# Optimization experiments

Measured on AMD Instinct MI355X. Metric: run time of the kernel, lower is better.

The kernel has to match this reference:

```python
import jax, jax.numpy as jnp
import numpy as np

EPS = 1e-12
RANK = 16


def setup_inputs() -> dict:
    key = jax.random.key(0)
    ks = jax.random.split(key, 7)
    bs, seq, d_in, d_out = 8, 2048, 4096, 4096
    n_tasks, n_splits, n_skills, rank = 256, 1, 8, RANK
    return {
        "x": jax.random.normal(ks[0], (bs, seq, d_in), dtype=jnp.float32),
        "task_ids": jax.random.randint(ks[1], (bs,), 0, n_tasks, dtype=jnp.int64 if jax.config.jax_enable_x64 else jnp.int32),
        "weight": jax.random.normal(ks[2], (d_out, d_in), dtype=jnp.float32) * 0.02,
        "bias": jax.random.normal(ks[3], (d_out,), dtype=jnp.float32) * 0.02,
        "module_logits": jax.random.normal(ks[4], (n_tasks, n_splits * n_skills), dtype=jnp.float32) * 0.001,
        "lora_a": jax.random.normal(ks[5], (n_splits, n_skills, d_in // n_splits, rank), dtype=jnp.float32) * 0.01,
        "lora_b": jax.random.normal(ks[6], (n_splits, n_skills, rank, d_out // n_splits), dtype=jnp.float32) * 0.01,
    }


def reference(x, task_ids, weight, bias, module_logits, lora_a, lora_b):
    bs = x.shape[0]
    n_splits, n_skills, _, rank = lora_a.shape
    d_in = n_splits * lora_a.shape[2]
    d_out = n_splits * lora_b.shape[3]
    # PolytroponSelector (eval path): sigmoid then sum-normalize over skills
    logits = module_logits[task_ids].reshape(bs, n_splits, n_skills)
    mw = jax.nn.sigmoid(logits)
    mw = mw / (mw.sum(axis=-1, keepdims=True) + EPS)  # [b, q, s]
    # Mix LoRA skill matrices per example
    A = jnp.einsum('bqs,qsdr->bqdr', mw, lora_a).reshape(bs, d_in, rank)
    B = jnp.einsum('bqs,qsrd->bqrd', mw, lora_b)
    B = jnp.transpose(B, (0, 2, 1, 3)).reshape(bs, rank, d_out)
    adapter_out = jnp.einsum('btr,brd->btd', jnp.einsum('bti,bir->btr', x, A), B) / rank
    base = jnp.einsum('bti,oi->bto', x, weight) + bias
    return base + adapter_out
```

## Files before the change

### kernel.cpp

```cpp
#include <hip/hip_runtime.h>
#include <hip/hip_bf16.h>
#include <cstdint>
#include <cstddef>

typedef __bf16 bf16_t;
typedef __bf16 bf16x8 __attribute__((ext_vector_type(8)));
typedef float f32x4 __attribute__((ext_vector_type(4)));

#define GLP(p)  (const __attribute__((address_space(1))) void*)(p)
#define LDSP(p) (__attribute__((address_space(3))) void*)(p)

static constexpr int BS   = 8;
static constexpr int SEQ  = 2048;
static constexpr int DIN  = 4096;
static constexpr int DOUT = 4096;
static constexpr int NSK  = 8;
static constexpr int RANK = 16;
static constexpr int MTOT = BS * SEQ;
static constexpr int NKT  = 128;

static __device__ __forceinline__ bf16x8 cvt8(float4 v0, float4 v1) {
    bf16x8 o;
    o[0] = (bf16_t)v0.x; o[1] = (bf16_t)v0.y; o[2] = (bf16_t)v0.z; o[3] = (bf16_t)v0.w;
    o[4] = (bf16_t)v1.x; o[5] = (bf16_t)v1.y; o[6] = (bf16_t)v1.z; o[7] = (bf16_t)v1.w;
    return o;
}

__global__ __launch_bounds__(256) void mix_kernel(
    const float* __restrict__ logits, const int* __restrict__ task_ids,
    const float* __restrict__ lora_a, const float* __restrict__ lora_b,
    bf16_t* __restrict__ Abt, bf16_t* __restrict__ Btp) {
    int b = blockIdx.y;
    int c = blockIdx.x;
    int tid = threadIdx.x;

    int t = task_ids[b];
    float w[NSK]; float sum = 0.f;
#pragma unroll
    for (int s = 0; s < NSK; ++s) {
        float lg = logits[t * NSK + s];
        float sg = 1.f / (1.f + __expf(-lg));
        w[s] = sg; sum += sg;
    }
    float inv = 1.f / (sum + 1e-12f);
#pragma unroll
    for (int s = 0; s < NSK; ++s) w[s] *= inv;

    {
        int r = tid & 15, kk = tid >> 4;
#pragma unroll
        for (int i = 0; i < 4; ++i) {
            int k = c * 64 + i * 16 + kk;
            float acc = 0.f;
#pragma unroll
            for (int s = 0; s < NSK; ++s)
                acc += w[s] * lora_a[((size_t)s * DIN + k) * RANK + r];
            Abt[((size_t)b * RANK + r) * DIN + k] = (bf16_t)acc;
        }
    }
    {
        int n = c * 64 + (tid & 63);
        int r0 = tid >> 6;
#pragma unroll
        for (int i = 0; i < 4; ++i) {
            int rr = r0 + i * 4;
            float acc = 0.f;
#pragma unroll
            for (int s = 0; s < NSK; ++s)
                acc += w[s] * lora_b[((size_t)s * RANK + rr) * DOUT + n];
            Btp[((size_t)b * DOUT + n) * 32 + rr] = (bf16_t)acc;
            Btp[((size_t)b * DOUT + n) * 32 + 16 + rr] = (bf16_t)0.f;
        }
    }
}

__global__ __launch_bounds__(256) void convw_kernel(const float* __restrict__ W,
                                                    bf16_t* __restrict__ Wb) {
    size_t g = (size_t)blockIdx.x * 256 + threadIdx.x;
    const float4* src = (const float4*)W;
    float4 v0 = src[g * 2], v1 = src[g * 2 + 1];
    *(bf16x8*)(Wb + g * 8) = cvt8(v0, v1);
}

template<bool XPRE>
__global__ __launch_bounds__(256) void tconv_kernel(
    const float* __restrict__ x, const bf16_t* __restrict__ Abt,
    bf16_t* __restrict__ xb, bf16_t* __restrict__ tpad) {
    __shared__ __align__(16) bf16_t As[64 * 64];
    __shared__ __align__(16) bf16_t Aa[16 * 64];

    int row0 = blockIdx.x * 64;
    int b = row0 >> 11;
    int tid = threadIdx.x;
    int w = tid >> 6, l = tid & 63;
    const bf16_t* Ab = Abt + (size_t)b * RANK * DIN;

    f32x4 acc = {0.f, 0.f, 0.f, 0.f};

    for (int k0 = 0; k0 < DIN; k0 += 64) {
#pragma unroll
        for (int i = 0; i < 2; ++i) {
            int flat = i * 256 + tid;
            int row = flat >> 3, c8 = flat & 7;
            const float* src = x + (size_t)(row0 + row) * DIN + k0 + c8 * 8;
            float4 v0 = *(const float4*)src;
            float4 v1 = *(const float4*)(src + 4);
            bf16x8 o = cvt8(v0, v1);
            *(bf16x8*)(&As[flat * 8]) = o;
            if (XPRE)
                *(bf16x8*)(xb + (size_t)(row0 + row) * DIN + k0 + c8 * 8) = o;
        }
        if (tid < 128) {
            int r = tid >> 3, c8 = tid & 7;
            __builtin_amdgcn_global_load_lds(GLP(Ab + (size_t)r * DIN + k0 + c8 * 8),
                                             LDSP(&Aa[tid * 8]), 16, 0, 0);
        }
        __syncthreads();
#pragma unroll
        for (int s = 0; s < 2; ++s) {
            int kr = s * 32 + (l >> 4) * 8;
            bf16x8 a = *(const bf16x8*)(&As[(w * 16 + (l & 15)) * 64 + kr]);
            bf16x8 bb = *(const bf16x8*)(&Aa[(l & 15) * 64 + kr]);
            acc = __builtin_amdgcn_mfma_f32_16x16x32_bf16(a, bb, acc, 0, 0, 0);
        }
        __syncthreads();
    }
    int r = l & 15;
    int rowb = w * 16 + (l >> 4) * 4;
#pragma unroll
    for (int j = 0; j < 4; ++j) {
        int gm = row0 + rowb + j;
        tpad[(size_t)gm * 32 + r] = (bf16_t)(acc[j] * 0.0625f);
        tpad[(size_t)gm * 32 + 16 + r] = (bf16_t)0.f;
    }
}

#define SBAR   __builtin_amdgcn_s_barrier()
#define SCHEDB __builtin_amdgcn_sched_barrier(0)
#define VMG(TXT) asm volatile("s_waitcnt " TXT ::: "memory")

__global__ __launch_bounds__(256, 2) void gemm3_kernel(
    const bf16_t* __restrict__ xb, const bf16_t* __restrict__ Wb,
    const float* __restrict__ bias,
    const bf16_t* __restrict__ tpad, const bf16_t* __restrict__ Btp,
    float* __restrict__ out) {
    __shared__ __align__(16) bf16_t lds[2][12288];

    int tid = threadIdx.x;
    int w = tid >> 6, l = tid & 63;
    int wm = w >> 1, wn = w & 1;
    int l4 = l >> 4, l15 = l & 15;

    int orig = blockIdx.x;
    int id = (orig & 7) * 256 + (orig >> 3);
    int mb = id >> 5, nb = id & 31;
    int row0 = mb * 256, col0 = nb * 128;
    int b = row0 >> 11;

    f32x4 acc[8][4] = {};

    auto stageA = [&](const bf16_t* base, size_t rstride, int c) {
#pragma unroll
        for (int ld = 0; ld < 4; ++ld) {
            int flat = ld * 256 + tid;
            int r = flat >> 2, ch = flat & 3;
            int sc = ch ^ (r & 3);
            __builtin_amdgcn_global_load_lds(
                GLP(base + (size_t)r * rstride + sc * 8),
                LDSP(&lds[c][flat * 8]), 16, 0, 0);
        }
    };
    auto stageB = [&](const bf16_t* base, size_t rstride, int c) {
#pragma unroll
        for (int ld = 0; ld < 2; ++ld) {
            int flat = ld * 256 + tid;
            int r = flat >> 2, ch = flat & 3;
            int sc = ch ^ (r & 3);
            __builtin_amdgcn_global_load_lds(
                GLP(base + (size_t)r * rstride + sc * 8),
                LDSP(&lds[c][8192 + flat * 8]), 16, 0, 0);
        }
    };

    auto loadAfrag = [&](int c, int i) {
        int row = wm * 128 + i * 16 + l15;
        return *(const bf16x8*)(&lds[c][row * 32 + ((l4 ^ (row & 3)) << 3)]);
    };
    auto loadBfrag = [&](int c, int jj) {
        int row = wn * 64 + jj * 16 + l15;
        return *(const bf16x8*)(&lds[c][8192 + row * 32 + ((l4 ^ (row & 3)) << 3)]);
    };

    const bf16_t* Abase = xb + (size_t)row0 * DIN;
    const bf16_t* Bbase = Wb + (size_t)col0 * DIN;
    const bf16_t* AbaseAdp = tpad + (size_t)row0 * 32;
    const bf16_t* BbaseAdp = Btp + ((size_t)b * DOUT + col0) * 32;

    stageA(Abase, DIN, 0);
    stageB(Bbase, DIN, 0);

#pragma unroll 1
    for (int j = 0; j <= NKT; ++j) {
        int c = j & 1;
        SCHEDB; SBAR; SCHEDB;
        if (j < NKT) {
            int jn = j + 1;
            if (jn < NKT) stageA(Abase + jn * 32, DIN, c ^ 1);
            else          stageA(AbaseAdp, 32, c ^ 1);
            VMG("vmcnt(4)");
        } else {
            VMG("vmcnt(0)");
        }
        SCHEDB;
        SBAR; SCHEDB;

        bf16x8 a0[4], a1[4], b0[2], b1[2];
#pragma unroll
        for (int i = 0; i < 4; ++i) a0[i] = loadAfrag(c, i);
#pragma unroll
        for (int jj = 0; jj < 2; ++jj) b0[jj] = loadBfrag(c, jj);
        if (j < NKT) {
            int jn = j + 1;
            if (jn < NKT) stageB(Bbase + jn * 32, DIN, c ^ 1);
            else          stageB(BbaseAdp, 32, c ^ 1);
        }
#pragma unroll
        for (int i = 0; i < 4; ++i)
#pragma unroll
            for (int jj = 0; jj < 2; ++jj)
                acc[i][jj] = __builtin_amdgcn_mfma_f32_16x16x32_bf16(
                    a0[i], b0[jj], acc[i][jj], 0, 0, 0);
#pragma unroll
        for (int jj = 0; jj < 2; ++jj) b1[jj] = loadBfrag(c, 2 + jj);
#pragma unroll
        for (int i = 0; i < 4; ++i)
#pragma unroll
            for (int jj = 0; jj < 2; ++jj)
                acc[i][2 + jj] = __builtin_amdgcn_mfma_f32_16x16x32_bf16(
                    a0[i], b1[jj], acc[i][2 + jj], 0, 0, 0);
#pragma unroll
        for (int i = 0; i < 4; ++i) a1[i] = loadAfrag(c, 4 + i);
#pragma unroll
        for (int i = 0; i < 4; ++i)
#pragma unroll
            for (int jj = 0; jj < 2; ++jj)
                acc[4 + i][2 + jj] = __builtin_amdgcn_mfma_f32_16x16x32_bf16(
                    a1[i], b1[jj], acc[4 + i][2 + jj], 0, 0, 0);
#pragma unroll
        for (int i = 0; i < 4; ++i)
#pragma unroll
            for (int jj = 0; jj < 2; ++jj)
                acc[4 + i][jj] = __builtin_amdgcn_mfma_f32_16x16x32_bf16(
                    a1[i], b0[jj], acc[4 + i][jj], 0, 0, 0);
    }

#pragma unroll
    for (int i = 0; i < 8; ++i) {
        int gm = row0 + wm * 128 + i * 16 + l4 * 4;
#pragma unroll
        for (int jj = 0; jj < 4; ++jj) {
            int gn = col0 + wn * 64 + jj * 16 + l15;
            float bsv = bias[gn];
#pragma unroll
            for (int q = 0; q < 4; ++q)
                out[(size_t)(gm + q) * DOUT + gn] = acc[i][jj][q] + bsv;
        }
    }
}

template<bool WPRE>
__global__ __launch_bounds__(256) void gemm_kernel(
    const float* __restrict__ xf,
    const float* __restrict__ Wf, const bf16_t* __restrict__ Wb,
    const float* __restrict__ bias,
    const bf16_t* __restrict__ tpad, const bf16_t* __restrict__ Btp,
    float* __restrict__ out) {
    __shared__ __align__(16) bf16_t As[128 * 64];
    __shared__ __align__(16) bf16_t Bs[128 * 64];

    int orig = blockIdx.x;
    int id = (orig & 7) * 512 + (orig >> 3);
    int mb = id >> 5, nb = id & 31;
    int row0 = mb * 128, col0 = nb * 128;
    int b = row0 >> 11;

    int tid = threadIdx.x;
    int w = tid >> 6, l = tid & 63;
    int wm = w >> 1, wn = w & 1;

    f32x4 acc[4][4] = {};

    for (int k0 = 0; k0 < DIN; k0 += 64) {
#pragma unroll
        for (int i = 0; i < 4; ++i) {
            int flat = i * 256 + tid;
            int row = flat >> 3, c8 = flat & 7;
            const float* src = xf + (size_t)(row0 + row) * DIN + k0 + c8 * 8;
            float4 v0 = *(const float4*)src;
            float4 v1 = *(const float4*)(src + 4);
            *(bf16x8*)(&As[flat * 8]) = cvt8(v0, v1);
        }
        if constexpr (WPRE) {
#pragma unroll
            for (int i = 0; i < 4; ++i) {
                int flat = i * 256 + tid;
                int row = flat >> 3, c8 = flat & 7;
                __builtin_amdgcn_global_load_lds(
                    GLP(Wb + (size_t)(col0 + row) * DIN + k0 + c8 * 8),
                    LDSP(&Bs[flat * 8]), 16, 0, 0);
            }
        } else {
#pragma unroll
            for (int i = 0; i < 4; ++i) {
                int flat = i * 256 + tid;
                int row = flat >> 3, c8 = flat & 7;
                const float* src = Wf + (size_t)(col0 + row) * DIN + k0 + c8 * 8;
                float4 v0 = *(const float4*)src;
                float4 v1 = *(const float4*)(src + 4);
                *(bf16x8*)(&Bs[flat * 8]) = cvt8(v0, v1);
            }
        }
        __syncthreads();
#pragma unroll
        for (int s = 0; s < 2; ++s) {
            int kr = s * 32 + (l >> 4) * 8;
            bf16x8 a[4], bf[4];
#pragma unroll
            for (int i = 0; i < 4; ++i)
                a[i] = *(const bf16x8*)(&As[(wm * 64 + i * 16 + (l & 15)) * 64 + kr]);
#pragma unroll
            for (int j = 0; j < 4; ++j)
                bf[j] = *(const bf16x8*)(&Bs[(wn * 64 + j * 16 + (l & 15)) * 64 + kr]);
#pragma unroll
            for (int i = 0; i < 4; ++i)
#pragma unroll
                for (int j = 0; j < 4; ++j)
                    acc[i][j] = __builtin_amdgcn_mfma_f32_16x16x32_bf16(a[i], bf[j], acc[i][j], 0, 0, 0);
        }
        __syncthreads();
    }

    {
#pragma unroll
        for (int i = 0; i < 2; ++i) {
            int flat = i * 256 + tid;
            int row = flat >> 2, c8 = flat & 3;
            __builtin_amdgcn_global_load_lds(
                GLP(tpad + (size_t)(row0 + row) * 32 + c8 * 8),
                LDSP(&As[flat * 8]), 16, 0, 0);
            __builtin_amdgcn_global_load_lds(
                GLP(Btp + ((size_t)b * DOUT + col0 + row) * 32 + c8 * 8),
                LDSP(&Bs[flat * 8]), 16, 0, 0);
        }
        __syncthreads();
        int kr = (l >> 4) * 8;
        bf16x8 a[4], bf[4];
#pragma unroll
        for (int i = 0; i < 4; ++i)
            a[i] = *(const bf16x8*)(&As[(wm * 64 + i * 16 + (l & 15)) * 32 + kr]);
#pragma unroll
        for (int j = 0; j < 4; ++j)
            bf[j] = *(const bf16x8*)(&Bs[(wn * 64 + j * 16 + (l & 15)) * 32 + kr]);
#pragma unroll
        for (int i = 0; i < 4; ++i)
#pragma unroll
            for (int j = 0; j < 4; ++j)
                acc[i][j] = __builtin_amdgcn_mfma_f32_16x16x32_bf16(a[i], bf[j], acc[i][j], 0, 0, 0);
    }

#pragma unroll
    for (int i = 0; i < 4; ++i) {
        int gm = row0 + wm * 64 + i * 16 + (l >> 4) * 4;
#pragma unroll
        for (int j = 0; j < 4; ++j) {
            int gn = col0 + wn * 64 + j * 16 + (l & 15);
            float bs = bias[gn];
#pragma unroll
            for (int q = 0; q < 4; ++q)
                out[(size_t)(gm + q) * DOUT + gn] = acc[i][j][q] + bs;
        }
    }
}

extern "C" void kernel_launch(void* const* d_in, const int* in_sizes, int n_in,
                              void* d_out, int out_size, void* d_ws, size_t ws_size,
                              hipStream_t stream) {
    const float* x        = (const float*)d_in[0];
    const int*   task_ids = (const int*)d_in[1];
    const float* W        = (const float*)d_in[2];
    const float* bias     = (const float*)d_in[3];
    const float* logits   = (const float*)d_in[4];
    const float* lora_a   = (const float*)d_in[5];
    const float* lora_b   = (const float*)d_in[6];
    float* out = (float*)d_out;

    char* ws = (char*)d_ws;
    size_t off = 0;
    auto alloc = [&](size_t bytes) {
        char* p = ws + off;
        off += (bytes + 255) & ~(size_t)255;
        return p;
    };
    bf16_t* Abt  = (bf16_t*)alloc((size_t)BS * RANK * DIN * 2);
    bf16_t* Btp  = (bf16_t*)alloc((size_t)BS * DOUT * 32 * 2);
    bf16_t* tpad = (bf16_t*)alloc((size_t)MTOT * 32 * 2);
    bf16_t* Wb   = (bf16_t*)alloc((size_t)DOUT * DIN * 2);
    size_t w_end = off;
    bf16_t* xb   = (bf16_t*)alloc((size_t)MTOT * DIN * 2);
    size_t full_end = off;

    bool wpre = ws_size >= w_end;
    bool xpre = ws_size >= full_end;

    mix_kernel<<<dim3(64, 8), 256, 0, stream>>>(logits, task_ids, lora_a, lora_b, Abt, Btp);
    if (wpre)
        convw_kernel<<<(DOUT * DIN / 8) / 256, 256, 0, stream>>>(W, Wb);
    if (xpre)
        tconv_kernel<true><<<MTOT / 64, 256, 0, stream>>>(x, Abt, xb, tpad);
    else
        tconv_kernel<false><<<MTOT / 64, 256, 0, stream>>>(x, Abt, nullptr, tpad);

    if (xpre) {
        int nblk = (MTOT / 256) * (DOUT / 128);
        gemm3_kernel<<<nblk, 256, 0, stream>>>(xb, Wb, bias, tpad, Btp, out);
    } else {
        int nblk = (MTOT / 128) * (DOUT / 128);
        if (wpre)
            gemm_kernel<true><<<nblk, 256, 0, stream>>>(x, W, Wb, bias, tpad, Btp, out);
        else
            gemm_kernel<false><<<nblk, 256, 0, stream>>>(x, W, Wb, bias, tpad, Btp, out);
    }
}
```

Before: 687.0 us.

## Restructure main GEMM to 512 threads, BK=64, triple-buffered LDS pipeline

The bf16 GEMM kernel goes from 256 to 512 threads per block, so each wave holds a 64x64 sub-tile instead of 128x64. The K step doubles to 64 with an 8-chunk XOR swizzle, and a three-deep LDS ring replaces the double buffer, with loads issued two stages ahead. The adapter rank pass becomes a separate epilogue MFMA step. The aim is to halve the barriers per K, hide more global latency and lower per-thread register pressure, at the cost of more LDS (about 144KB per block), which may limit occupancy to one block per CU.

```diff
diff --git a/kernel.cpp b/kernel.cpp
--- a/kernel.cpp
+++ b/kernel.cpp
@@ -17,7 +17,6 @@
 static constexpr int NSK  = 8;
 static constexpr int RANK = 16;
 static constexpr int MTOT = BS * SEQ;
-static constexpr int NKT  = 128;
 
 static __device__ __forceinline__ bf16x8 cvt8(float4 v0, float4 v1) {
     bf16x8 o;
@@ -139,12 +138,13 @@
 #define SCHEDB __builtin_amdgcn_sched_barrier(0)
 #define VMG(TXT) asm volatile("s_waitcnt " TXT ::: "memory")
 
-__global__ __launch_bounds__(256, 2) void gemm3_kernel(
+__global__ __launch_bounds__(512, 2) void gemm3_kernel(
     const bf16_t* __restrict__ xb, const bf16_t* __restrict__ Wb,
     const float* __restrict__ bias,
     const bf16_t* __restrict__ tpad, const bf16_t* __restrict__ Btp,
     float* __restrict__ out) {
-    __shared__ __align__(16) bf16_t lds[2][12288];
+    __shared__ __align__(16) bf16_t bufA[3][256 * 64];
+    __shared__ __align__(16) bf16_t bufB[3][128 * 64];
 
     int tid = threadIdx.x;
     int w = tid >> 6, l = tid & 63;
@@ -157,106 +157,156 @@
     int row0 = mb * 256, col0 = nb * 128;
     int b = row0 >> 11;
 
-    f32x4 acc[8][4] = {};
-
-    auto stageA = [&](const bf16_t* base, size_t rstride, int c) {
+    f32x4 acc[4][4] = {};
+
+    const bf16_t* aSrc[4];
+    const bf16_t* bSrc[2];
+#pragma unroll
+    for (int ld = 0; ld < 4; ++ld) {
+        int flat = ld * 512 + tid;
+        int r = flat >> 3;
+        int sc = (flat & 7) ^ (r & 7);
+        aSrc[ld] = xb + (size_t)(row0 + r) * DIN + sc * 8;
+    }
+#pragma unroll
+    for (int ld = 0; ld < 2; ++ld) {
+        int flat = ld * 512 + tid;
+        int r = flat >> 3;
+        int sc = (flat & 7) ^ (r & 7);
+        bSrc[ld] = Wb + (size_t)(col0 + r) * DIN + sc * 8;
+    }
+
+    auto stage = [&](int t) {
+        int c = t % 3;
+        int k0 = t * 64;
 #pragma unroll
         for (int ld = 0; ld < 4; ++ld) {
-            int flat = ld * 256 + tid;
-            int r = flat >> 2, ch = flat & 3;
-            int sc = ch ^ (r & 3);
+            int flat = ld * 512 + tid;
+            __builtin_amdgcn_global_load_lds(GLP(aSrc[ld] + k0),
+                                             LDSP(&bufA[c][flat * 8]), 16, 0, 0);
+        }
+#pragma unroll
+        for (int ld = 0; ld < 2; ++ld) {
+            int flat = ld * 512 + tid;
+            __builtin_amdgcn_global_load_lds(GLP(bSrc[ld] + k0),
+                                             LDSP(&bufB[c][flat * 8]), 16, 0, 0);
+        }
+    };
+    auto stageAdp = [&]() {
+#pragma unroll
+        for (int ld = 0; ld < 2; ++ld) {
+            int flat = ld * 512 + tid;
+            int r = flat >> 2, c4 = flat & 3;
             __builtin_amdgcn_global_load_lds(
-                GLP(base + (size_t)r * rstride + sc * 8),
-                LDSP(&lds[c][flat * 8]), 16, 0, 0);
+                GLP(tpad + (size_t)(row0 + r) * 32 + c4 * 8),
+                LDSP(&bufA[1][flat * 8]), 16, 0, 0);
+        }
+        {
+            int r = tid >> 2, c4 = tid & 3;
+            __builtin_amdgcn_global_load_lds(
+                GLP(Btp + ((size_t)b * DOUT + col0 + r) * 32 + c4 * 8),
+                LDSP(&bufB[1][tid * 8]), 16, 0, 0);
         }
     };
-    auto stageB = [&](const bf16_t* base, size_t rstride, int c) {
-#pragma unroll
-        for (int ld = 0; ld < 2; ++ld) {
-            int flat = ld * 256 + tid;
-            int r = flat >> 2, ch = flat & 3;
-            int sc = ch ^ (r & 3);
-            __builtin_amdgcn_global_load_lds(
-                GLP(base + (size_t)r * rstride + sc * 8),
-                LDSP(&lds[c][8192 + flat * 8]), 16, 0, 0);
-        }
+
+    auto loadAfrag = [&](int c, int i, int s) {
+        int row = wm * 64 + i * 16 + l15;
+        int ch = (s * 4 + l4) ^ (row & 7);
+        return *(const bf16x8*)(&bufA[c][row * 64 + ch * 8]);
     };
-
-    auto loadAfrag = [&](int c, int i) {
-        int row = wm * 128 + i * 16 + l15;
-        return *(const bf16x8*)(&lds[c][row * 32 + ((l4 ^ (row & 3)) << 3)]);
+    auto loadBfrag = [&](int c, int jj, int s) {
+        int row = wn * 64 + jj * 16 + l15;
+        int ch = (s * 4 + l4) ^ (row & 7);
+        return *(const bf16x8*)(&bufB[c][row * 64 + ch * 8]);
     };
-    auto loadBfrag = [&](int c, int jj) {
-        int row = wn * 64 + jj * 16 + l15;
-        return *(const bf16x8*)(&lds[c][8192 + row * 32 + ((l4 ^ (row & 3)) << 3)]);
-    };
-
-    const bf16_t* Abase = xb + (size_t)row0 * DIN;
-    const bf16_t* Bbase = Wb + (size_t)col0 * DIN;
-    const bf16_t* AbaseAdp = tpad + (size_t)row0 * 32;
-    const bf16_t* BbaseAdp = Btp + ((size_t)b * DOUT + col0) * 32;
-
-    stageA(Abase, DIN, 0);
-    stageB(Bbase, DIN, 0);
+
+    stage(0);
+    stage(1);
 
 #pragma unroll 1
-    for (int j = 0; j <= NKT; ++j) {
-        int c = j & 1;
+    for (int j = 0; j < 64; ++j) {
+        int c = j % 3;
         SCHEDB; SBAR; SCHEDB;
-        if (j < NKT) {
-            int jn = j + 1;
-            if (jn < NKT) stageA(Abase + jn * 32, DIN, c ^ 1);
-            else          stageA(AbaseAdp, 32, c ^ 1);
-            VMG("vmcnt(4)");
-        } else {
-            VMG("vmcnt(0)");
-        }
+        if (j < 62)       stage(j + 2);
+        else if (j == 62) stageAdp();
+        if (j < 63) { VMG("vmcnt(6)"); } else { VMG("vmcnt(3)"); }
         SCHEDB;
-        SBAR; SCHEDB;
-
-        bf16x8 a0[4], a1[4], b0[2], b1[2];
-#pragma unroll
-        for (int i = 0; i < 4; ++i) a0[i] = loadAfrag(c, i);
-#pragma unroll
-        for (int jj = 0; jj < 2; ++jj) b0[jj] = loadBfrag(c, jj);
-        if (j < NKT) {
-            int jn = j + 1;
-            if (jn < NKT) stageB(Bbase + jn * 32, DIN, c ^ 1);
-            else          stageB(BbaseAdp, 32, c ^ 1);
+
+        bf16x8 aL[2][2], aH[2][2], bL[2][2], bH[2][2];
+#pragma unroll
+        for (int i = 0; i < 2; ++i)
+#pragma unroll
+            for (int s = 0; s < 2; ++s) aL[i][s] = loadAfrag(c, i, s);
+#pragma unroll
+        for (int jj = 0; jj < 2; ++jj)
+#pragma unroll
+            for (int s = 0; s < 2; ++s) bL[jj][s] = loadBfrag(c, jj, s);
+#pragma unroll
+        for (int s = 0; s < 2; ++s)
+#pragma unroll
+            for (int i = 0; i < 2; ++i)
+#pragma unroll
+                for (int jj = 0; jj < 2; ++jj)
+                    acc[i][jj] = __builtin_amdgcn_mfma_f32_16x16x32_bf16(
+                        aL[i][s], bL[jj][s], acc[i][jj], 0, 0, 0);
+#pragma unroll
+        for (int jj = 0; jj < 2; ++jj)
+#pragma unroll
+            for (int s = 0; s < 2; ++s) bH[jj][s] = loadBfrag(c, 2 + jj, s);
+#pragma unroll
+        for (int s = 0; s < 2; ++s)
+#pragma unroll
+            for (int i = 0; i < 2; ++i)
+#pragma unroll
+                for (int jj = 0; jj < 2; ++jj)
+                    acc[i][2 + jj] = __builtin_amdgcn_mfma_f32_16x16x32_bf16(
+                        aL[i][s], bH[jj][s], acc[i][2 + jj], 0, 0, 0);
+#pragma unroll
+        for (int i = 0; i < 2; ++i)
+#pragma unroll
+            for (int s = 0; s < 2; ++s) aH[i][s] = loadAfrag(c, 2 + i, s);
+#pragma unroll
+        for (int s = 0; s < 2; ++s)
+#pragma unroll
+            for (int i = 0; i < 2; ++i)
+#pragma unroll
+                for (int jj = 0; jj < 2; ++jj)
+                    acc[2 + i][2 + jj] = __builtin_amdgcn_mfma_f32_16x16x32_bf16(
+                        aH[i][s], bH[jj][s], acc[2 + i][2 + jj], 0, 0, 0);
+#pragma unroll
+        for (int s = 0; s < 2; ++s)
+#pragma unroll
+            for (int i = 0; i < 2; ++i)
+#pragma unroll
+                for (int jj = 0; jj < 2; ++jj)
+                    acc[2 + i][jj] = __builtin_amdgcn_mfma_f32_16x16x32_bf16(
+                        aH[i][s], bL[jj][s], acc[2 + i][jj], 0, 0, 0);
+    }
+
+    VMG("vmcnt(0)"); SCHEDB; SBAR; SCHEDB;
+    {
+        bf16x8 aa[4], bb[4];
+#pragma unroll
+        for (int i = 0; i < 4; ++i) {
+            int row = wm * 64 + i * 16 + l15;
+            aa[i] = *(const bf16x8*)(&bufA[1][row * 32 + l4 * 8]);
+        }
+#pragma unroll
+        for (int jj = 0; jj < 4; ++jj) {
+            int row = wn * 64 + jj * 16 + l15;
+            bb[jj] = *(const bf16x8*)(&bufB[1][row * 32 + l4 * 8]);
         }
 #pragma unroll
         for (int i = 0; i < 4; ++i)
 #pragma unroll
-            for (int jj = 0; jj < 2; ++jj)
+            for (int jj = 0; jj < 4; ++jj)
                 acc[i][jj] = __builtin_amdgcn_mfma_f32_16x16x32_bf16(
-                    a0[i], b0[jj], acc[i][jj], 0, 0, 0);
-#pragma unroll
-        for (int jj = 0; jj < 2; ++jj) b1[jj] = loadBfrag(c, 2 + jj);
-#pragma unroll
-        for (int i = 0; i < 4; ++i)
-#pragma unroll
-            for (int jj = 0; jj < 2; ++jj)
-                acc[i][2 + jj] = __builtin_amdgcn_mfma_f32_16x16x32_bf16(
-                    a0[i], b1[jj], acc[i][2 + jj], 0, 0, 0);
-#pragma unroll
-        for (int i = 0; i < 4; ++i) a1[i] = loadAfrag(c, 4 + i);
-#pragma unroll
-        for (int i = 0; i < 4; ++i)
-#pragma unroll
-            for (int jj = 0; jj < 2; ++jj)
-                acc[4 + i][2 + jj] = __builtin_amdgcn_mfma_f32_16x16x32_bf16(
-                    a1[i], b1[jj], acc[4 + i][2 + jj], 0, 0, 0);
-#pragma unroll
-        for (int i = 0; i < 4; ++i)
-#pragma unroll
-            for (int jj = 0; jj < 2; ++jj)
-                acc[4 + i][jj] = __builtin_amdgcn_mfma_f32_16x16x32_bf16(
-                    a1[i], b0[jj], acc[4 + i][jj], 0, 0, 0);
-    }
-
-#pragma unroll
-    for (int i = 0; i < 8; ++i) {
-        int gm = row0 + wm * 128 + i * 16 + l4 * 4;
+                    aa[i], bb[jj], acc[i][jj], 0, 0, 0);
+    }
+
+#pragma unroll
+    for (int i = 0; i < 4; ++i) {
+        int gm = row0 + wm * 64 + i * 16 + l4 * 4;
 #pragma unroll
         for (int jj = 0; jj < 4; ++jj) {
             int gn = col0 + wn * 64 + jj * 16 + l15;
@@ -422,7 +472,7 @@
 
     if (xpre) {
         int nblk = (MTOT / 256) * (DOUT / 128);
-        gemm3_kernel<<<nblk, 256, 0, stream>>>(xb, Wb, bias, tpad, Btp, out);
+        gemm3_kernel<<<nblk, 512, 0, stream>>>(xb, Wb, bias, tpad, Btp, out);
     } else {
         int nblk = (MTOT / 128) * (DOUT / 128);
         if (wpre)
```

Result: slower. 985.7 us (+43.5%).
